# Performance work log

Measured on AMD Instinct MI355X. Metric: run time of the kernel, lower is better.

## Reference

```python
import jax, jax.numpy as jnp
import numpy as np

NUM_CLASSES = 10000
FEAT_DIM = 1024
BATCH = 4096


def setup_inputs() -> dict:
    key = jax.random.key(0)
    k1, k2 = jax.random.split(key)
    feat = jax.random.normal(k1, (BATCH, FEAT_DIM), dtype=jnp.float32)
    centers = jax.random.normal(k2, (NUM_CLASSES, FEAT_DIM), dtype=jnp.float32)
    return {"feat": feat, "centers": centers}


def reference(feat, centers):
    # logits = -0.5 * ||feat_b - center_c||^2, computed via the GEMM rewrite
    # ||a-b||^2 = ||a||^2 + ||b||^2 - 2 a.b  (same math as broadcast-sub-square-sum,
    # but avoids the [B, C, D] intermediate and uses tensor-core matmul).
    feat_sq = jnp.sum(feat * feat, axis=-1, keepdims=True)          # [B, 1]
    cent_sq = jnp.sum(centers * centers, axis=-1)[None, :]          # [1, C]
    cross = jnp.einsum('bd,cd->bc', feat, centers)                  # [B, C]
    dist = feat_sq + cent_sq - 2.0 * cross                          # [B, C]
    logits = -0.5 * dist
    return logits
```

## Files before the change

### kernel.cpp

```cpp
#include <hip/hip_runtime.h>
#include <hip/hip_bf16.h>
#include <stdint.h>

#define M_DIM 4096
#define N_DIM 10000
#define K_DIM 1024
#define GM (M_DIM / 256)
#define GN ((N_DIM + 255) / 256)
#define NT (K_DIM / 32)

typedef __attribute__((ext_vector_type(8))) short bf16x8;
typedef __attribute__((ext_vector_type(4))) float f32x4;

#define BAR()      asm volatile("s_barrier" ::: "memory")
#define WAITVM8()  asm volatile("s_waitcnt vmcnt(8)" ::: "memory")
#define WAITVM4()  asm volatile("s_waitcnt vmcnt(4)" ::: "memory")
#define WAITVM0()  asm volatile("s_waitcnt vmcnt(0)" ::: "memory")
#define WAITLGKM() asm volatile("s_waitcnt lgkmcnt(0)" ::: "memory")

__device__ __forceinline__ void async_ld16(const void* g, void* l) {
    __builtin_amdgcn_global_load_lds(
        (const __attribute__((address_space(1))) unsigned int*)g,
        (__attribute__((address_space(3))) unsigned int*)l,
        16, 0, 0);
}

__device__ __forceinline__ unsigned short f2bf(float f) {
    unsigned u = __float_as_uint(f);
    unsigned r = (u + 0x7FFFu + ((u >> 16) & 1u)) >> 16;
    return (unsigned short)r;
}

__global__ __launch_bounds__(256) void prep_rows(
    const float* __restrict__ feat, const float* __restrict__ cent,
    unsigned short* __restrict__ featbf, unsigned short* __restrict__ centbf,
    float* __restrict__ fsq, float* __restrict__ csq)
{
    const int wlane = threadIdx.x & 63;
    const int wid   = blockIdx.x * 4 + (threadIdx.x >> 6);
    const int nw    = gridDim.x * 4;
    for (int row = wid; row < M_DIM + N_DIM; row += nw) {
        const float* in;
        unsigned short* outb;
        float* sqp;
        if (row < M_DIM) {
            in = feat + (size_t)row * K_DIM;
            outb = featbf + (size_t)row * K_DIM;
            sqp = fsq + row;
        } else {
            const int r2 = row - M_DIM;
            in = cent + (size_t)r2 * K_DIM;
            outb = centbf + (size_t)r2 * K_DIM;
            sqp = csq + r2;
        }
        float s = 0.f;
        #pragma unroll
        for (int c = 0; c < 4; c++) {
            float4 v = ((const float4*)in)[wlane + c * 64];
            ushort4 pk;
            pk.x = f2bf(v.x); pk.y = f2bf(v.y); pk.z = f2bf(v.z); pk.w = f2bf(v.w);
            ((ushort4*)outb)[wlane + c * 64] = pk;
            s += v.x * v.x + v.y * v.y + v.z * v.z + v.w * v.w;
        }
        #pragma unroll
        for (int off = 32; off > 0; off >>= 1) s += __shfl_down(s, off, 64);
        if (wlane == 0) *sqp = s;
    }
}

__global__ __launch_bounds__(512, 2) void gemm_bt(
    const unsigned short* __restrict__ A,
    const unsigned short* __restrict__ B,
    const float* __restrict__ fsq, const float* __restrict__ csq,
    float* __restrict__ out)
{
    __shared__ unsigned short smem[65536];

    const int tid  = threadIdx.x;
    const int lane = tid & 63;
    const int wave = tid >> 6;
    const int wm = wave & 1;
    const int wn = wave >> 1;
    const int mlane = lane & 15;
    const int quad  = lane >> 4;
    const int fr  = (mlane >> 1) & 3;
    const int qx  = (quad ^ fr) << 4;

    const int bid = blockIdx.x;
    const int xcd = bid & 7;
    const int idx = bid >> 3;
    const int r0  = xcd * 80 + idx;
    const int bm  = r0 & 15;
    const int bn  = r0 >> 4;

    const int arow_base = bm * 256;
    const int brow_base = bn * 256;

    const unsigned short* gA[2];
    const unsigned short* gB[2];
    int ldsA[2], ldsB[2];
    #pragma unroll
    for (int i = 0; i < 2; i++) {
        const int s   = i * 512 + tid;
        const int row = s >> 2;
        const int sc  = s & 3;
        const int kof = (sc ^ ((row >> 1) & 3)) << 3;
        gA[i] = A + (size_t)(arow_base + row) * K_DIM + kof;
        int br = brow_base + row; if (br > N_DIM - 1) br = N_DIM - 1;
        gB[i] = B + (size_t)br * K_DIM + kof;
        ldsA[i] = s * 16;
        ldsB[i] = 16384 + s * 16;
    }

    #define STAGE_A(t2, nbb)                                                  \
        do {                                                                  \
            async_ld16(gA[0] + (size_t)(t2) * 32, (char*)smem + (nbb) + ldsA[0]); \
            async_ld16(gA[1] + (size_t)(t2) * 32, (char*)smem + (nbb) + ldsA[1]); \
        } while (0)
    #define STAGE_B(t2, nbb)                                                  \
        do {                                                                  \
            async_ld16(gB[0] + (size_t)(t2) * 32, (char*)smem + (nbb) + ldsB[0]); \
            async_ld16(gB[1] + (size_t)(t2) * 32, (char*)smem + (nbb) + ldsB[1]); \
        } while (0)

    f32x4 acc[8][4];
    #pragma unroll
    for (int i = 0; i < 8; i++)
        #pragma unroll
        for (int j = 0; j < 4; j++) {
            f32x4 z = {0.f, 0.f, 0.f, 0.f};
            acc[i][j] = z;
        }

    const int aBase = (wm * 128 + mlane) * 64 + qx;
    const int bBase = 16384 + (wn * 64 + mlane) * 64 + qx;

    STAGE_A(0, 0);     STAGE_B(0, 0);
    STAGE_A(1, 32768); STAGE_B(1, 32768);
    STAGE_A(2, 65536); STAGE_B(2, 65536);
    WAITVM8();
    BAR();

    for (int t = 0; t < NT; ++t) {
        const int bb = (t & 3) * 32768;
        const int nb = ((t + 3) & 3) * 32768;
        const char* base = (const char*)smem + bb;
        bf16x8 af[4], bfv[4];

        #pragma unroll
        for (int i = 0; i < 4; i++) {
            af[i]  = *(const bf16x8*)(base + aBase + i * 1024);
            bfv[i] = *(const bf16x8*)(base + bBase + i * 1024);
        }
        if (t + 3 < NT) STAGE_A(t + 3, nb);
        __builtin_amdgcn_s_setprio(1);
        #pragma unroll
        for (int i = 0; i < 4; i++)
            #pragma unroll
            for (int j = 0; j < 4; j++)
                acc[i][j] = __builtin_amdgcn_mfma_f32_16x16x32_bf16(
                    af[i], bfv[j], acc[i][j], 0, 0, 0);
        __builtin_amdgcn_s_setprio(0);
        BAR();

        #pragma unroll
        for (int i = 0; i < 4; i++)
            af[i] = *(const bf16x8*)(base + aBase + 4096 + i * 1024);
        if (t + 3 < NT) STAGE_B(t + 3, nb);
        __builtin_amdgcn_s_setprio(1);
        #pragma unroll
        for (int i = 0; i < 4; i++)
            #pragma unroll
            for (int j = 0; j < 4; j++)
                acc[4 + i][j] = __builtin_amdgcn_mfma_f32_16x16x32_bf16(
                    af[i], bfv[j], acc[4 + i][j], 0, 0, 0);
        __builtin_amdgcn_s_setprio(0);

        if (t < NT - 1) {
            if (t < NT - 3)      { WAITVM8(); }
            else if (t == NT - 3){ WAITVM4(); }
            else                 { WAITVM0(); }
        }
        BAR();
    }
    #undef STAGE_A
    #undef STAGE_B

    float* W = (float*)smem + wave * 1088;
    const int rbase0 = arow_base + wm * 128;
    const int cbase  = brow_base + wn * 64 + mlane;
    const int rb_col4 = mlane * 4;
    const int gcol4  = brow_base + wn * 64 + rb_col4;
    const bool colok = gcol4 < N_DIM;

    #pragma unroll
    for (int i = 0; i < 8; i++) {
        float frow[4];
        #pragma unroll
        for (int r = 0; r < 4; r++)
            frow[r] = -0.5f * fsq[rbase0 + i * 16 + quad * 4 + r];
        #pragma unroll
        for (int j = 0; j < 4; j++) {
            int col = cbase + j * 16;
            float cs = -0.5f * csq[col < N_DIM ? col : (N_DIM - 1)];
            #pragma unroll
            for (int r = 0; r < 4; r++)
                W[(quad * 4 + r) * 68 + j * 16 + mlane] = acc[i][j][r] + frow[r] + cs;
        }
        WAITLGKM();
        #pragma unroll
        for (int s = 0; s < 4; s++) {
            int rl = s * 4 + quad;
            f32x4 v = *(const f32x4*)&W[rl * 68 + rb_col4];
            if (colok) {
                int grow = rbase0 + i * 16 + rl;
                __builtin_nontemporal_store(v, (f32x4*)&out[(size_t)grow * N_DIM + gcol4]);
            }
        }
        WAITLGKM();
    }
}

extern "C" void kernel_launch(void* const* d_in, const int* in_sizes, int n_in,
                              void* d_out, int out_size, void* d_ws, size_t ws_size,
                              hipStream_t stream) {
    const float* feat = (const float*)d_in[0];
    const float* cent = (const float*)d_in[1];
    float* out = (float*)d_out;

    char* ws = (char*)d_ws;
    unsigned short* featbf = (unsigned short*)ws;
    unsigned short* centbf = (unsigned short*)(ws + 8388608);
    float* fsq = (float*)(ws + 8388608 + 20480000);
    float* csq = (float*)(ws + 8388608 + 20480000 + 16384);

    prep_rows<<<1024, 256, 0, stream>>>(feat, cent, featbf, centbf, fsq, csq);

    gemm_bt<<<GM * GN, 512, 0, stream>>>(featbf, centbf, fsq, csq, out);
}
```

Measured before the change: 287.9 us.

## Shrink GEMM tile to 128x128 with 4 waves and double buffering

Replaces the 256x256 block tile, which used 8 waves and a 4-stage async LDS pipeline, with a 128x128 tile that uses 4 waves, a simple double-buffered pipeline and 4 blocks per CU. The aim is to raise occupancy and even out load across CUs by launching many more, smaller blocks, cutting the tail imbalance of the 640-block grid. In exchange, each block does less reuse of global loads and gets less arithmetic per LDS read. There is also less prefetch depth to hide memory latency, and a barrier runs every k-step.

```diff
diff --git a/kernel.cpp b/kernel.cpp
--- a/kernel.cpp
+++ b/kernel.cpp
@@ -5,15 +5,14 @@
 #define M_DIM 4096
 #define N_DIM 10000
 #define K_DIM 1024
-#define GM (M_DIM / 256)
-#define GN ((N_DIM + 255) / 256)
+#define GM (M_DIM / 128)
+#define GN ((N_DIM + 127) / 128)
 #define NT (K_DIM / 32)
 
 typedef __attribute__((ext_vector_type(8))) short bf16x8;
 typedef __attribute__((ext_vector_type(4))) float f32x4;
 
 #define BAR()      asm volatile("s_barrier" ::: "memory")
-#define WAITVM8()  asm volatile("s_waitcnt vmcnt(8)" ::: "memory")
 #define WAITVM4()  asm volatile("s_waitcnt vmcnt(4)" ::: "memory")
 #define WAITVM0()  asm volatile("s_waitcnt vmcnt(0)" ::: "memory")
 #define WAITLGKM() asm volatile("s_waitcnt lgkmcnt(0)" ::: "memory")
@@ -68,13 +67,13 @@
     }
 }
 
-__global__ __launch_bounds__(512, 2) void gemm_bt(
+__global__ __launch_bounds__(256, 4) void gemm_bt(
     const unsigned short* __restrict__ A,
     const unsigned short* __restrict__ B,
     const float* __restrict__ fsq, const float* __restrict__ csq,
     float* __restrict__ out)
 {
-    __shared__ unsigned short smem[65536];
+    __shared__ unsigned short smem[16384];
 
     const int tid  = threadIdx.x;
     const int lane = tid & 63;
@@ -83,25 +82,24 @@
     const int wn = wave >> 1;
     const int mlane = lane & 15;
     const int quad  = lane >> 4;
-    const int fr  = (mlane >> 1) & 3;
-    const int qx  = (quad ^ fr) << 4;
+    const int qx  = (quad ^ ((mlane >> 1) & 3)) << 4;
 
     const int bid = blockIdx.x;
     const int xcd = bid & 7;
     const int idx = bid >> 3;
-    const int r0  = xcd * 80 + idx;
-    const int bm  = r0 & 15;
-    const int bn  = r0 >> 4;
-
-    const int arow_base = bm * 256;
-    const int brow_base = bn * 256;
+    const int r0  = xcd * 316 + idx;
+    const int bm  = r0 & 31;
+    const int bn  = r0 >> 5;
+
+    const int arow_base = bm * 128;
+    const int brow_base = bn * 128;
 
     const unsigned short* gA[2];
     const unsigned short* gB[2];
     int ldsA[2], ldsB[2];
     #pragma unroll
     for (int i = 0; i < 2; i++) {
-        const int s   = i * 512 + tid;
+        const int s   = i * 256 + tid;
         const int row = s >> 2;
         const int sc  = s & 3;
         const int kof = (sc ^ ((row >> 1) & 3)) << 3;
@@ -109,50 +107,44 @@
         int br = brow_base + row; if (br > N_DIM - 1) br = N_DIM - 1;
         gB[i] = B + (size_t)br * K_DIM + kof;
         ldsA[i] = s * 16;
-        ldsB[i] = 16384 + s * 16;
-    }
-
-    #define STAGE_A(t2, nbb)                                                  \
+        ldsB[i] = 8192 + s * 16;
+    }
+
+    #define STAGE(t2, nbb)                                                    \
         do {                                                                  \
             async_ld16(gA[0] + (size_t)(t2) * 32, (char*)smem + (nbb) + ldsA[0]); \
             async_ld16(gA[1] + (size_t)(t2) * 32, (char*)smem + (nbb) + ldsA[1]); \
-        } while (0)
-    #define STAGE_B(t2, nbb)                                                  \
-        do {                                                                  \
             async_ld16(gB[0] + (size_t)(t2) * 32, (char*)smem + (nbb) + ldsB[0]); \
             async_ld16(gB[1] + (size_t)(t2) * 32, (char*)smem + (nbb) + ldsB[1]); \
         } while (0)
 
-    f32x4 acc[8][4];
+    f32x4 acc[4][4];
     #pragma unroll
-    for (int i = 0; i < 8; i++)
+    for (int i = 0; i < 4; i++)
         #pragma unroll
         for (int j = 0; j < 4; j++) {
             f32x4 z = {0.f, 0.f, 0.f, 0.f};
             acc[i][j] = z;
         }
 
-    const int aBase = (wm * 128 + mlane) * 64 + qx;
-    const int bBase = 16384 + (wn * 64 + mlane) * 64 + qx;
-
-    STAGE_A(0, 0);     STAGE_B(0, 0);
-    STAGE_A(1, 32768); STAGE_B(1, 32768);
-    STAGE_A(2, 65536); STAGE_B(2, 65536);
-    WAITVM8();
-    BAR();
+    const int aBase = (wm * 64 + mlane) * 64 + qx;
+    const int bBase = 8192 + (wn * 64 + mlane) * 64 + qx;
+
+    STAGE(0, 0);
 
     for (int t = 0; t < NT; ++t) {
-        const int bb = (t & 3) * 32768;
-        const int nb = ((t + 3) & 3) * 32768;
-        const char* base = (const char*)smem + bb;
+        const char* base = (const char*)smem + (t & 1) * 16384;
+        const int  nb    = ((t + 1) & 1) * 16384;
+        if (t + 1 < NT) { STAGE(t + 1, nb); WAITVM4(); }
+        else            { WAITVM0(); }
+        BAR();
+
         bf16x8 af[4], bfv[4];
-
         #pragma unroll
         for (int i = 0; i < 4; i++) {
             af[i]  = *(const bf16x8*)(base + aBase + i * 1024);
             bfv[i] = *(const bf16x8*)(base + bBase + i * 1024);
         }
-        if (t + 3 < NT) STAGE_A(t + 3, nb);
         __builtin_amdgcn_s_setprio(1);
         #pragma unroll
         for (int i = 0; i < 4; i++)
@@ -162,39 +154,18 @@
                     af[i], bfv[j], acc[i][j], 0, 0, 0);
         __builtin_amdgcn_s_setprio(0);
         BAR();
-
-        #pragma unroll
-        for (int i = 0; i < 4; i++)
-            af[i] = *(const bf16x8*)(base + aBase + 4096 + i * 1024);
-        if (t + 3 < NT) STAGE_B(t + 3, nb);
-        __builtin_amdgcn_s_setprio(1);
-        #pragma unroll
-        for (int i = 0; i < 4; i++)
-            #pragma unroll
-            for (int j = 0; j < 4; j++)
-                acc[4 + i][j] = __builtin_amdgcn_mfma_f32_16x16x32_bf16(
-                    af[i], bfv[j], acc[4 + i][j], 0, 0, 0);
-        __builtin_amdgcn_s_setprio(0);
-
-        if (t < NT - 1) {
-            if (t < NT - 3)      { WAITVM8(); }
-            else if (t == NT - 3){ WAITVM4(); }
-            else                 { WAITVM0(); }
-        }
-        BAR();
-    }
-    #undef STAGE_A
-    #undef STAGE_B
+    }
+    #undef STAGE
 
     float* W = (float*)smem + wave * 1088;
-    const int rbase0 = arow_base + wm * 128;
+    const int rbase0 = arow_base + wm * 64;
     const int cbase  = brow_base + wn * 64 + mlane;
     const int rb_col4 = mlane * 4;
     const int gcol4  = brow_base + wn * 64 + rb_col4;
     const bool colok = gcol4 < N_DIM;
 
     #pragma unroll
-    for (int i = 0; i < 8; i++) {
+    for (int i = 0; i < 4; i++) {
         float frow[4];
         #pragma unroll
         for (int r = 0; r < 4; r++)
@@ -236,5 +207,5 @@
 
     prep_rows<<<1024, 256, 0, stream>>>(feat, cent, featbf, centbf, fsq, csq);
 
-    gemm_bt<<<GM * GN, 512, 0, stream>>>(featbf, centbf, fsq, csq, out);
-}
+    gemm_bt<<<GM * GN, 256, 0, stream>>>(featbf, centbf, fsq, csq, out);
+}
```

New measurement: 303.6 us. +5.4%, slower.
